# Kernel tuning notes

Measured on AMD Instinct MI355X. Metric: run time of the kernel, lower is better.

The kernel has to match this reference:

```python
import jax, jax.numpy as jnp
import numpy as np
import math

B, S, F, D, H, L, E, K = 8, 1024, 8, 512, 8, 3, 4, 2
HD = D // H


def _ln(x, g, b, eps=1e-5):
    m = x.mean(-1, keepdims=True)
    v = x.var(-1, keepdims=True)
    return (x - m) / jnp.sqrt(v + eps) * g + b


def _pos_encoding(seq, d):
    pos = jnp.arange(seq, dtype=jnp.float32)[:, None]
    div = jnp.exp(jnp.arange(0, d, 2, dtype=jnp.float32) * (-math.log(10000.0) / d))
    pe = jnp.zeros((seq, d), jnp.float32)
    pe = pe.at[:, 0::2].set(jnp.sin(pos * div))
    pe = pe.at[:, 1::2].set(jnp.cos(pos * div))
    return pe


def setup_inputs() -> dict:
    key = jax.random.key(0)
    ks = iter(jax.random.split(key, 40))

    def w(shape, s=0.02):
        return jax.random.normal(next(ks), shape, jnp.float32) * s

    return {
        "x": jax.random.normal(next(ks), (B, S, F), jnp.float32),
        "Wp": w((D, F)), "bp": jnp.zeros((D,), jnp.float32),
        "femb": w((5, D)),
        "qkv_w": w((L, 3 * D, D)), "qkv_b": jnp.zeros((L, 3 * D), jnp.float32),
        "ow": w((L, D, D)), "ob": jnp.zeros((L, D), jnp.float32),
        "g1": jnp.ones((L, D), jnp.float32), "beta1": jnp.zeros((L, D), jnp.float32),
        "gw": w((L, E, D)), "gb": jnp.zeros((L, E), jnp.float32),
        "ew1": w((L, E, 2 * D, D)), "eb1": jnp.zeros((L, E, 2 * D), jnp.float32),
        "ew2": w((L, E, D, 2 * D)), "eb2": jnp.zeros((L, E, D), jnp.float32),
        "g2": jnp.ones((L, D), jnp.float32), "beta2": jnp.zeros((L, D), jnp.float32),
        "hw": w((3, D)), "hb": jnp.zeros((3,), jnp.float32),
        "freq_idx": 2,
    }


def reference(x, Wp, bp, femb, qkv_w, qkv_b, ow, ob, g1, beta1, gw, gb,
              ew1, eb1, ew2, eb2, g2, beta2, hw, hb, freq_idx):
    # instance norm over time axis (torch std is unbiased -> ddof=1)
    mean = x.mean(axis=1, keepdims=True)
    std = x.std(axis=1, ddof=1, keepdims=True) + 1e-5
    xn = (x - mean) / std

    h = xn @ Wp.T + bp                      # [B,S,D]
    h = h + femb[freq_idx]                  # broadcast freq embedding
    h = h + _pos_encoding(S, D)

    for l in range(L):
        # --- multi-head self-attention ---
        qkv = h @ qkv_w[l].T + qkv_b[l]     # [B,S,3D]
        q, k, v = jnp.split(qkv, 3, axis=-1)
        q = q.reshape(B, S, H, HD).transpose(0, 2, 1, 3)
        k = k.reshape(B, S, H, HD).transpose(0, 2, 1, 3)
        v = v.reshape(B, S, H, HD).transpose(0, 2, 1, 3)
        att = jax.nn.softmax(jnp.einsum('bhqd,bhkd->bhqk', q, k) / math.sqrt(HD), axis=-1)
        o = jnp.einsum('bhqk,bhkd->bhqd', att, v).transpose(0, 2, 1, 3).reshape(B, S, D)
        o = o @ ow[l].T + ob[l]
        h = _ln(h + o, g1[l], beta1[l])

        # --- SparseMoE: top-k softmax gating, renormalized combine ---
        flat = h.reshape(-1, D)                               # [T,D], T=B*S
        probs = jax.nn.softmax(flat @ gw[l].T + gb[l], axis=-1)
        tw, ti = jax.lax.top_k(probs, K)                      # [T,K]
        tw = tw / tw.sum(axis=-1, keepdims=True)
        hid = jax.nn.relu(jnp.einsum('td,efd->tef', flat, ew1[l]) + eb1[l])  # [T,E,2D]
        eo = jnp.einsum('tef,edf->ted', hid, ew2[l]) + eb2[l]                # [T,E,D]
        cw = (jax.nn.one_hot(ti, E, dtype=flat.dtype) * tw[..., None]).sum(1)  # [T,E]
        moe = jnp.einsum('te,ted->td', cw, eo).reshape(B, S, D)
        h = _ln(h + moe, g2[l], beta2[l])

    return h[:, -1, :] @ hw.T + hb           # [B,3] quantiles
```

## Files before the change

kernel.cpp:

```cpp
#include <hip/hip_runtime.h>
#include <hip/hip_bf16.h>
#include <math.h>

typedef __hip_bfloat16 bf16;
typedef __attribute__((ext_vector_type(8))) short short8;
typedef __attribute__((ext_vector_type(4))) short s4v;
typedef __attribute__((ext_vector_type(4))) float f32x4;

constexpr int B_ = 8, S_ = 1024, F_ = 8, D_ = 512, H_ = 8, E_ = 4;
constexpr int T_  = B_ * S_;
constexpr int D3_ = 3 * D_;
constexpr int CAP_ = T_ * 2 + E_ * 128;

__device__ __forceinline__ float b2f(bf16 v) { return __bfloat162float(v); }
__device__ __forceinline__ float ldin(const void* p, size_t i, int bf) {
  return bf ? __bfloat162float(((const bf16*)p)[i]) : ((const float*)p)[i];
}
__device__ __forceinline__ void gload16(const void* g, void* l) {
  __builtin_amdgcn_global_load_lds((const __attribute__((address_space(1))) unsigned int*)g,
                                   (__attribute__((address_space(3))) unsigned int*)l, 16, 0, 0);
}

__global__ void detect_kernel(const void* __restrict__ x, int* __restrict__ flag) {
  if (threadIdx.x == 0 && blockIdx.x == 0) {
    const unsigned short* u = (const unsigned short*)x;
    int c = 0;
    for (int i = 0; i < 256; i += 2) {
      int ex = (u[i] >> 7) & 0xFF;
      if (ex >= 96 && ex <= 144) c++;
    }
    flag[0] = (c >= 64) ? 1 : 0;
  }
}

__global__ __launch_bounds__(256) void convw_kernel(const void* __restrict__ Asrc, size_t offA,
                                                    size_t nA,
                                                    const void* __restrict__ Bsrc, size_t offB,
                                                    bf16* __restrict__ dst,
                                                    const int* __restrict__ flag) {
  const int bf = flag[0];
  size_t i = ((size_t)blockIdx.x * 256 + threadIdx.x) * 8;
  const void* s = Asrc;
  size_t so = offA + i;
  if (i >= nA) { s = Bsrc; so = offB + (i - nA); }
  if (bf) {
    *(short8*)(dst + i) = *(const short8*)((const bf16*)s + so);
  } else {
    const float* sp = (const float*)s + so;
    short8 v;
#pragma unroll
    for (int u = 0; u < 8; u++) { bf16 t = __float2bfloat16(sp[u]); v[u] = *(short*)&t; }
    *(short8*)(dst + i) = v;
  }
}

__global__ __launch_bounds__(256) void instnorm_kernel(const void* __restrict__ x,
                                                       float* __restrict__ xn,
                                                       const int* __restrict__ flag) {
  const int bf = flag[0];
  int b = blockIdx.x / F_, f = blockIdx.x % F_;
  int tid = threadIdx.x;
  __shared__ float red[256];
  const int base = b * S_ * F_ + f;
  float s = 0.f;
  for (int j = tid; j < S_; j += 256) s += ldin(x, base + j * F_, bf);
  red[tid] = s; __syncthreads();
  for (int w = 128; w; w >>= 1) { if (tid < w) red[tid] += red[tid + w]; __syncthreads(); }
  float mean = red[0] / S_;
  __syncthreads();
  float v = 0.f;
  for (int j = tid; j < S_; j += 256) { float d = ldin(x, base + j * F_, bf) - mean; v += d * d; }
  red[tid] = v; __syncthreads();
  for (int w = 128; w; w >>= 1) { if (tid < w) red[tid] += red[tid + w]; __syncthreads(); }
  float inv = 1.f / (sqrtf(red[0] / (float)(S_ - 1)) + 1e-5f);
  for (int j = tid; j < S_; j += 256) xn[base + j * F_] = (ldin(x, base + j * F_, bf) - mean) * inv;
}

__global__ __launch_bounds__(256) void pe_kernel(const void* __restrict__ bp,
                                                 const void* __restrict__ femb,
                                                 const int* __restrict__ freq_idx,
                                                 float* __restrict__ addtab,
                                                 const int* __restrict__ flag) {
  const int bf = flag[0];
  int idx = blockIdx.x * 256 + threadIdx.x;
  int dp = idx & (D_ / 2 - 1);
  int s  = idx / (D_ / 2);
  int d0 = dp * 2;
  int fi = freq_idx[0];
  const float cexp = -9.2103403719761836f / (float)D_;
  float ang = (float)s * expf((float)d0 * cexp);
  float sv, cv;
  sincosf(ang, &sv, &cv);
  addtab[(size_t)s * D_ + d0]     = sv + ldin(bp, d0, bf)     + ldin(femb, (size_t)fi * D_ + d0, bf);
  addtab[(size_t)s * D_ + d0 + 1] = cv + ldin(bp, d0 + 1, bf) + ldin(femb, (size_t)fi * D_ + d0 + 1, bf);
}

constexpr int IPG_ = 8;
__global__ __launch_bounds__(256) void input_proj_kernel(const float* __restrict__ xn,
                                                         const void* __restrict__ Wp,
                                                         const float* __restrict__ addtab,
                                                         float* __restrict__ h,
                                                         bf16* __restrict__ hb16,
                                                         const int* __restrict__ flag) {
  const int bf = flag[0];
  const int tid = threadIdx.x;
  const int d0 = tid * 2;
  const int tbase = blockIdx.x * IPG_;
  float wp0[8], wp1[8];
  if (bf) {
    short8 w0 = *(const short8*)((const bf16*)Wp + (size_t)d0 * F_);
    short8 w1 = *(const short8*)((const bf16*)Wp + (size_t)(d0 + 1) * F_);
#pragma unroll
    for (int f = 0; f < 8; f++) {
      unsigned short u0 = (unsigned short)w0[f], u1 = (unsigned short)w1[f];
      wp0[f] = __bfloat162float(*(bf16*)&u0);
      wp1[f] = __bfloat162float(*(bf16*)&u1);
    }
  } else {
    const float* wpf = (const float*)Wp + (size_t)d0 * F_;
    f32x4 a = *(const f32x4*)(wpf);
    f32x4 b = *(const f32x4*)(wpf + 4);
    f32x4 c = *(const f32x4*)(wpf + 8);
    f32x4 d = *(const f32x4*)(wpf + 12);
#pragma unroll
    for (int f = 0; f < 4; f++) { wp0[f] = a[f]; wp0[4 + f] = b[f]; wp1[f] = c[f]; wp1[4 + f] = d[f]; }
  }
#pragma unroll
  for (int g = 0; g < IPG_; g++) {
    int t = tbase + g;
    int s = t & (S_ - 1);
    const float* xr = xn + (size_t)t * F_;
    f32x4 x0 = *(const f32x4*)xr;
    f32x4 x1 = *(const f32x4*)(xr + 4);
    const float2 at = *(const float2*)(addtab + (size_t)s * D_ + d0);
    float a0 = at.x, a1 = at.y;
#pragma unroll
    for (int f = 0; f < 4; f++) { a0 += x0[f] * wp0[f]; a1 += x0[f] * wp1[f]; }
#pragma unroll
    for (int f = 0; f < 4; f++) { a0 += x1[f] * wp0[4 + f]; a1 += x1[f] * wp1[4 + f]; }
    *(float2*)(h + (size_t)t * D_ + d0) = make_float2(a0, a1);
    bf16 b0 = __float2bfloat16(a0), b1 = __float2bfloat16(a1);
    unsigned pk = (unsigned)(*(unsigned short*)&b0) | ((unsigned)(*(unsigned short*)&b1) << 16);
    *(unsigned*)(hb16 + (size_t)t * D_ + d0) = pk;
  }
}

template <int MODE>
__global__ __launch_bounds__(256) void mfma_gemm(
    const bf16* __restrict__ A, const bf16* __restrict__ Wt,
    const void* __restrict__ bias, size_t boff, void* __restrict__ C_,
    int Kd, int lda, int ldb, int ldc, const int* __restrict__ flag) {
  const int wbf = flag[0];
  __shared__ bf16 As[3][128][32];
  __shared__ bf16 Bs[3][128][32];
  const int tid = threadIdx.x;
  const int ln = tid & 63, wv = tid >> 6;
  int id = blockIdx.x + gridDim.x * blockIdx.y;
  int xcd = id & 7, idq = id >> 3;
  const int n0 = (idq % gridDim.x) * 128;
  const int m0 = (xcd + 8 * (idq / gridDim.x)) * 128;
  const int wr = (wv >> 1) * 64, wc = (wv & 1) * 64;
  const int mrow = ln & 15, quad = ln >> 4;
  const int srow = ln >> 2;
  const int skof = (ln & 3) * 8;
  const int kchunk = Kd / gridDim.z;
  const int kbeg = blockIdx.z * kchunk;
  const int kend = kbeg + kchunk;

  auto stage = [&](int pb, int k0) {
#pragma unroll
    for (int j = 0; j < 2; j++) {
      int row = 16 * (4 * j + wv) + srow;
      gload16(A + (size_t)(m0 + row) * lda + k0 + skof,
              (char*)&As[pb][0][0] + (size_t)(4 * j + wv) * 1024);
    }
#pragma unroll
    for (int j = 0; j < 2; j++) {
      int row = 16 * (4 * j + wv) + srow;
      gload16(Wt + (size_t)(n0 + row) * ldb + k0 + skof,
              (char*)&Bs[pb][0][0] + (size_t)(4 * j + wv) * 1024);
    }
  };

  f32x4 acc[4][4];
#pragma unroll
  for (int i = 0; i < 4; i++)
#pragma unroll
    for (int j = 0; j < 4; j++) acc[i][j] = (f32x4){0.f, 0.f, 0.f, 0.f};

  stage(0, kbeg);
  stage(1, kbeg + 32);
  int p = 0;
  for (int k0 = kbeg; k0 < kend; k0 += 32) {
    if (k0 + 32 < kend) asm volatile("s_waitcnt vmcnt(4)" ::: "memory");
    else                asm volatile("s_waitcnt vmcnt(0)" ::: "memory");
    __builtin_amdgcn_s_barrier();
    __builtin_amdgcn_sched_barrier(0);
    short8 af[4], bfr[4];
#pragma unroll
    for (int t = 0; t < 4; t++) {
      af[t]  = *(const short8*)&As[p][wr + t * 16 + mrow][quad * 8];
      bfr[t] = *(const short8*)&Bs[p][wc + t * 16 + mrow][quad * 8];
    }
    if (k0 + 64 < kend) {
      int ps = (p == 0) ? 2 : p - 1;
      stage(ps, k0 + 64);
    }
#pragma unroll
    for (int i = 0; i < 4; i++)
#pragma unroll
      for (int j = 0; j < 4; j++)
        acc[i][j] = __builtin_amdgcn_mfma_f32_16x16x32_bf16(af[i], bfr[j], acc[i][j], 0, 0, 0);
    p = (p == 2) ? 0 : p + 1;
  }

  bf16* slice = (MODE == 0) ? (bf16*)C_ + (size_t)blockIdx.z * T_ * D_ : (bf16*)C_;
#pragma unroll
  for (int tj = 0; tj < 4; tj++) {
    int n = n0 + wc + tj * 16 + mrow;
    float bv = (MODE == 3) ? ldin(bias, boff + n, wbf) : 0.f;
#pragma unroll
    for (int ti = 0; ti < 4; ti++) {
      int mbase = m0 + wr + ti * 16 + quad * 4;
#pragma unroll
      for (int r = 0; r < 4; r++) {
        int m = mbase + r;
        float v = acc[ti][tj][r];
        slice[(size_t)m * ldc + n] = __float2bfloat16(MODE == 3 ? v + bv : v);
      }
    }
  }
}

__global__ __launch_bounds__(256) void attn_kernel(const bf16* __restrict__ qkv,
                                                   bf16* __restrict__ o) {
  __shared__ bf16 QP[64][72];
  __shared__ bf16 Ks[64][72];
  __shared__ bf16 Vt[64][72];
  const int tid = threadIdx.x;
  const int ln = tid & 63, wv = tid >> 6;
  const int mrow = ln & 15, quad = ln >> 4;
  const int id = blockIdx.x;
  const int xcd = id & 7, j = id >> 3;
  const int qt = j & 15;
  const int pr = xcd + 8 * (j >> 4);
  const int hh = pr & 7, b = pr >> 3;
  const int q0 = qt * 64;
  const int sr = tid >> 2;
  const int sg = tid & 3;
  const int sc = sg * 8;

  {
    const bf16* src = qkv + (size_t)(b * S_ + q0 + sr) * D3_ + hh * 64;
    *(short8*)&QP[sr][sc]      = *(const short8*)(src + sc);
    *(short8*)&QP[sr][sc + 32] = *(const short8*)(src + sc + 32);
  }
  __syncthreads();
  short8 aq[2];
  aq[0] = *(const short8*)&QP[wv * 16 + mrow][quad * 8];
  aq[1] = *(const short8*)&QP[wv * 16 + mrow][quad * 8 + 32];

  float m_st = -1e30f, l_st = 0.f;
  f32x4 oacc[4];
#pragma unroll
  for (int t = 0; t < 4; t++) oacc[t] = (f32x4){0.f, 0.f, 0.f, 0.f};

  for (int kt = 0; kt < 16; kt++) {
    int k0 = kt * 64;
    __syncthreads();
    {
      const bf16* src = qkv + (size_t)(b * S_ + k0 + sr) * D3_ + D_ + hh * 64;
      *(short8*)&Ks[sr][sc]      = *(const short8*)(src + sc);
      *(short8*)&Ks[sr][sc + 32] = *(const short8*)(src + sc + 32);
    }
    {
      const bf16* src = qkv + (size_t)(b * S_ + k0 + sr) * D3_ + 2 * D_ + hh * 64;
      short8 v0 = *(const short8*)(src + sc);
      short8 v1 = *(const short8*)(src + sc + 32);
      int col0 = sr ^ (sg << 4);
      int col1 = sr ^ (((sg + 4) & 3) << 4);
#pragma unroll
      for (int u = 0; u < 8; u++) {
        *(short*)&Vt[sc + u][col0]      = v0[u];
        *(short*)&Vt[sc + 32 + u][col1] = v1[u];
      }
    }
    __syncthreads();
    f32x4 s[4];
#pragma unroll
    for (int t = 0; t < 4; t++) {
      s[t] = (f32x4){0.f, 0.f, 0.f, 0.f};
#pragma unroll
      for (int ks = 0; ks < 2; ks++) {
        short8 bk = *(const short8*)&Ks[t * 16 + mrow][quad * 8 + ks * 32];
        s[t] = __builtin_amdgcn_mfma_f32_16x16x32_bf16(bk, aq[ks], s[t], 0, 0, 0);
      }
    }
    float rm = s[0][0];
#pragma unroll
    for (int t = 0; t < 4; t++)
#pragma unroll
      for (int r = 0; r < 4; r++) rm = fmaxf(rm, s[t][r]);
    rm *= 0.125f;
    rm = fmaxf(rm, __shfl_xor(rm, 16, 64));
    rm = fmaxf(rm, __shfl_xor(rm, 32, 64));
    float mnew = fmaxf(m_st, rm);
    float alpha = __expf(m_st - mnew);
    m_st = mnew;
    float rs = 0.f;
#pragma unroll
    for (int t = 0; t < 4; t++) {
      s4v pk;
#pragma unroll
      for (int r = 0; r < 4; r++) {
        float p = __expf(s[t][r] * 0.125f - mnew);
        rs += p;
        bf16 tb = __float2bfloat16(p);
        pk[r] = *(short*)&tb;
      }
      *(s4v*)&QP[wv * 16 + mrow][t * 16 + quad * 4] = pk;
    }
    rs += __shfl_xor(rs, 16, 64);
    rs += __shfl_xor(rs, 32, 64);
    l_st = l_st * alpha + rs;
    float af4[4];
#pragma unroll
    for (int r = 0; r < 4; r++) af4[r] = __shfl(alpha, quad * 4 + r, 64);
#pragma unroll
    for (int t = 0; t < 4; t++)
#pragma unroll
      for (int r = 0; r < 4; r++) oacc[t][r] *= af4[r];
    short8 ap[2];
    ap[0] = *(const short8*)&QP[wv * 16 + mrow][quad * 8];
    ap[1] = *(const short8*)&QP[wv * 16 + mrow][quad * 8 + 32];
#pragma unroll
    for (int t = 0; t < 4; t++) {
      int d = t * 16 + mrow;
      int swz = ((d >> 3) & 3) << 4;
#pragma unroll
      for (int ks = 0; ks < 2; ks++) {
        short8 bv = *(const short8*)&Vt[d][(quad * 8 + ks * 32) ^ swz];
        oacc[t] = __builtin_amdgcn_mfma_f32_16x16x32_bf16(ap[ks], bv, oacc[t], 0, 0, 0);
      }
    }
  }
  float linv[4];
#pragma unroll
  for (int r = 0; r < 4; r++) linv[r] = 1.f / __shfl(l_st, quad * 4 + r, 64);
#pragma unroll
  for (int r = 0; r < 4; r++) {
    size_t base = (size_t)(b * S_ + q0 + wv * 16 + quad * 4 + r) * D_ + hh * 64;
#pragma unroll
    for (int t = 0; t < 4; t++)
      o[base + t * 16 + mrow] = __float2bfloat16(oacc[t][r] * linv[r]);
  }
}

__global__ __launch_bounds__(256) void reduce_ln_kernel(float* __restrict__ h,
                                                        bf16* __restrict__ hb16,
                                                        const bf16* __restrict__ ps,
                                                        int nsl, int mode,
                                                        const void* __restrict__ bias,
                                                        size_t boff,
                                                        const float* __restrict__ cw,
                                                        const void* __restrict__ eb2p,
                                                        size_t e2off,
                                                        const void* __restrict__ g,
                                                        const void* __restrict__ beta,
                                                        size_t off,
                                                        const int* __restrict__ flag) {
  const int bf = flag[0];
  int t = blockIdx.x, tid = threadIdx.x;
  __shared__ float r1[256], r2[256];
  const size_t base = (size_t)t * D_;
  float o0 = 0.f, o1 = 0.f;
  for (int s = 0; s < nsl; s++) {
    o0 += b2f(ps[(size_t)s * T_ * D_ + base + tid]);
    o1 += b2f(ps[(size_t)s * T_ * D_ + base + tid + 256]);
  }
  if (mode == 0) {
    o0 += ldin(bias, boff + tid, bf);
    o1 += ldin(bias, boff + tid + 256, bf);
  } else {
#pragma unroll
    for (int e = 0; e < 4; e++) {
      float w = cw[t * 4 + e];
      o0 += w * ldin(eb2p, e2off + e * D_ + tid, bf);
      o1 += w * ldin(eb2p, e2off + e * D_ + tid + 256, bf);
    }
  }
  float* hr = h + base;
  float v0 = hr[tid] + o0;
  float v1 = hr[tid + 256] + o1;
  r1[tid] = v0 + v1;
  r2[tid] = v0 * v0 + v1 * v1;
  __syncthreads();
  for (int w = 128; w; w >>= 1) { if (tid < w) { r1[tid] += r1[tid + w]; r2[tid] += r2[tid + w]; } __syncthreads(); }
  float mean = r1[0] * (1.f / D_);
  float var  = r2[0] * (1.f / D_) - mean * mean;
  float rstd = rsqrtf(var + 1e-5f);
  float n0 = (v0 - mean) * rstd * ldin(g, off + tid, bf) + ldin(beta, off + tid, bf);
  float n1 = (v1 - mean) * rstd * ldin(g, off + tid + 256, bf) + ldin(beta, off + tid + 256, bf);
  hr[tid] = n0;
  hr[tid + 256] = n1;
  hb16[base + tid] = __float2bfloat16(n0);
  hb16[base + tid + 256] = __float2bfloat16(n1);
}

__global__ __launch_bounds__(256) void gate_kernel(const float* __restrict__ hbuf,
                                                   const void* __restrict__ gw, size_t gwoff,
                                                   const void* __restrict__ gb, size_t gboff,
                                                   float* __restrict__ cw,
                                                   int* __restrict__ einfo,
                                                   float* __restrict__ w0a,
                                                   float* __restrict__ w1a,
                                                   const int* __restrict__ flag) {
  const int bf = flag[0];
  int lane = threadIdx.x & 63, wv = threadIdx.x >> 6;
  int t = blockIdx.x * 4 + wv;
  const float* xr = hbuf + (size_t)t * D_;
  float a[4] = {0, 0, 0, 0};
  for (int d = lane; d < D_; d += 64) {
    float xv = xr[d];
#pragma unroll
    for (int e = 0; e < 4; e++) a[e] += xv * ldin(gw, gwoff + e * D_ + d, bf);
  }
#pragma unroll
  for (int e = 0; e < 4; e++)
    for (int off = 32; off; off >>= 1) a[e] += __shfl_xor(a[e], off, 64);
  if (lane == 0) {
    float lg[4];
#pragma unroll
    for (int e = 0; e < 4; e++) lg[e] = a[e] + ldin(gb, gboff + e, bf);
    float m = fmaxf(fmaxf(lg[0], lg[1]), fmaxf(lg[2], lg[3]));
    float p[4], s = 0.f;
#pragma unroll
    for (int e = 0; e < 4; e++) { p[e] = __expf(lg[e] - m); s += p[e]; }
#pragma unroll
    for (int e = 0; e < 4; e++) p[e] /= s;
    int i0 = 0;
    for (int e = 1; e < 4; e++) if (p[e] > p[i0]) i0 = e;
    int i1 = -1;
    for (int e = 0; e < 4; e++) if (e != i0 && (i1 < 0 || p[e] > p[i1])) i1 = e;
    float s2 = p[i0] + p[i1];
    float ww0 = p[i0] / s2, ww1 = p[i1] / s2;
    float outw[4] = {0, 0, 0, 0};
    outw[i0] = ww0; outw[i1] = ww1;
#pragma unroll
    for (int e = 0; e < 4; e++) cw[t * 4 + e] = outw[e];
    einfo[t] = i0 | (i1 << 4);
    w0a[t] = ww0; w1a[t] = ww1;
  }
}

__global__ __launch_bounds__(256) void route_scan_kernel(const int* __restrict__ einfo,
                                                         int* __restrict__ off,
                                                         int* __restrict__ endp,
                                                         int* __restrict__ cur,
                                                         int* __restrict__ tmap) {
  __shared__ int red[4][256];
  int tid = threadIdx.x;
  int c[4] = {0, 0, 0, 0};
  for (int t = tid; t < T_; t += 256) {
    int inf = einfo[t];
    c[inf & 15]++;
    c[(inf >> 4) & 15]++;
  }
#pragma unroll
  for (int e = 0; e < 4; e++) red[e][tid] = c[e];
  __syncthreads();
  for (int w = 128; w; w >>= 1) {
    if (tid < w)
#pragma unroll
      for (int e = 0; e < 4; e++) red[e][tid] += red[e][tid + w];
    __syncthreads();
  }
  if (tid == 0) {
    int o = 0, idx = 0;
#pragma unroll
    for (int e = 0; e < 4; e++) {
      int cnt = red[e][0];
      off[e] = o;
      endp[e] = o + cnt;
      cur[e] = 0;
      int nt = (cnt + 127) >> 7;
      for (int i = 0; i < nt; i++) tmap[1 + idx++] = e | (i << 8);
      o += nt << 7;
    }
    tmap[0] = idx;
  }
}

__global__ __launch_bounds__(256) void scatter_kernel(const int* __restrict__ einfo,
                                                      const float* __restrict__ w0a,
                                                      const float* __restrict__ w1a,
                                                      const int* __restrict__ off,
                                                      int* __restrict__ cur,
                                                      int* __restrict__ pack,
                                                      float* __restrict__ wlist) {
  int t = blockIdx.x * 256 + threadIdx.x;
  int lane = threadIdx.x & 63;
  int inf = einfo[t];
#pragma unroll
  for (int rank = 0; rank < 2; rank++) {
    int my_e = (rank == 0) ? (inf & 15) : ((inf >> 4) & 15);
    float w = (rank == 0) ? w0a[t] : w1a[t];
#pragma unroll
    for (int e = 0; e < 4; e++) {
      bool p = (my_e == e);
      unsigned long long mask = __ballot(p);
      if (!mask) continue;
      int leader = __ffsll((long long)mask) - 1;
      int base = 0;
      if (lane == leader) base = atomicAdd(&cur[e], (int)__popcll(mask));
      base = __shfl(base, leader, 64);
      if (p) {
        int pos = off[e] + base + (int)__popcll(mask & ((1ULL << lane) - 1ULL));
        pack[pos] = t * 2 + rank;
        wlist[pos] = w;
      }
    }
  }
}

__global__ __launch_bounds__(256) void moe_mat1_kernel(
    const bf16* __restrict__ A, const bf16* __restrict__ Wt,
    const void* __restrict__ bias, size_t boff, bf16* __restrict__ hid,
    const int* __restrict__ off, const int* __restrict__ endp,
    const int* __restrict__ pack, const float* __restrict__ wlist,
    const int* __restrict__ tmap, const int* __restrict__ flag) {
  const int wbf = flag[0];
  int id = blockIdx.x + 8 * blockIdx.y;
  int xcd = id & 7, idq = id >> 3;
  int wx = idq & 7, wy = xcd + 8 * (idq >> 3);
  if (wy >= tmap[0]) return;
  int ent = tmap[1 + wy];
  const int e = ent & 255, mt = ent >> 8;
  const int o = off[e], en = endp[e];
  const int n0 = wx * 128;
  __shared__ bf16 As[3][128][32];
  __shared__ bf16 Bs[3][128][32];
  const int tid = threadIdx.x;
  const int ln = tid & 63, wv = tid >> 6;
  const int m0 = o + mt * 128;
  const int wr = (wv >> 1) * 64, wc = (wv & 1) * 64;
  const int mrow = ln & 15, quad = ln >> 4;
  const int srow = ln >> 2;
  const int skof = (ln & 3) * 8;
  int tokr[2];
#pragma unroll
  for (int j = 0; j < 2; j++) {
    int pos = m0 + 16 * (4 * j + wv) + srow;
    tokr[j] = pack[min(pos, en - 1)] >> 1;
  }
  const size_t wbase = (size_t)e * 1024 * 512;

  auto stage = [&](int pb, int k0) {
#pragma unroll
    for (int j = 0; j < 2; j++)
      gload16(A + (size_t)tokr[j] * 512 + k0 + skof,
              (char*)&As[pb][0][0] + (size_t)(4 * j + wv) * 1024);
#pragma unroll
    for (int j = 0; j < 2; j++) {
      int row = 16 * (4 * j + wv) + srow;
      gload16(Wt + wbase + (size_t)(n0 + row) * 512 + k0 + skof,
              (char*)&Bs[pb][0][0] + (size_t)(4 * j + wv) * 1024);
    }
  };

  f32x4 acc[4][4];
#pragma unroll
  for (int i = 0; i < 4; i++)
#pragma unroll
    for (int j = 0; j < 4; j++) acc[i][j] = (f32x4){0.f, 0.f, 0.f, 0.f};

  stage(0, 0);
  stage(1, 32);
  int p = 0;
  for (int k0 = 0; k0 < 512; k0 += 32) {
    if (k0 + 32 < 512) asm volatile("s_waitcnt vmcnt(4)" ::: "memory");
    else               asm volatile("s_waitcnt vmcnt(0)" ::: "memory");
    __builtin_amdgcn_s_barrier();
    __builtin_amdgcn_sched_barrier(0);
    short8 af[4], bfr[4];
#pragma unroll
    for (int t = 0; t < 4; t++) {
      af[t]  = *(const short8*)&As[p][wr + t * 16 + mrow][quad * 8];
      bfr[t] = *(const short8*)&Bs[p][wc + t * 16 + mrow][quad * 8];
    }
    if (k0 + 64 < 512) {
      int ps = (p == 0) ? 2 : p - 1;
      stage(ps, k0 + 64);
    }
#pragma unroll
    for (int i = 0; i < 4; i++)
#pragma unroll
      for (int j = 0; j < 4; j++)
        acc[i][j] = __builtin_amdgcn_mfma_f32_16x16x32_bf16(af[i], bfr[j], acc[i][j], 0, 0, 0);
    p = (p == 2) ? 0 : p + 1;
  }

#pragma unroll
  for (int ti = 0; ti < 4; ti++) {
#pragma unroll
    for (int r = 0; r < 4; r++) {
      int pos = m0 + wr + ti * 16 + quad * 4 + r;
      float w = (pos < en) ? wlist[pos] : 0.f;
#pragma unroll
      for (int tj = 0; tj < 4; tj++) {
        int ncol = n0 + wc + tj * 16 + mrow;
        float v = acc[ti][tj][r] + ldin(bias, boff + e * 1024 + ncol, wbf);
        hid[(size_t)pos * 1024 + ncol] = __float2bfloat16(fmaxf(v, 0.f) * w);
      }
    }
  }
}

__global__ __launch_bounds__(256) void moe_mat2_kernel(
    const bf16* __restrict__ hid, const bf16* __restrict__ Wt,
    bf16* __restrict__ psl,
    const int* __restrict__ off, const int* __restrict__ endp,
    const int* __restrict__ pack, const int* __restrict__ tmap,
    const int* __restrict__ flag) {
  int id = blockIdx.x + 4 * blockIdx.y;
  int xcd = id & 7, idq = id >> 3;
  int wx = idq & 3, wy = xcd + 8 * (idq >> 2);
  if (wy >= tmap[0]) return;
  int ent = tmap[1 + wy];
  const int e = ent & 255, mt = ent >> 8;
  const int o = off[e], en = endp[e];
  const int n0 = wx * 128;
  __shared__ bf16 As[3][128][32];
  __shared__ bf16 Bs[3][128][32];
  const int tid = threadIdx.x;
  const int ln = tid & 63, wv = tid >> 6;
  const int m0 = o + mt * 128;
  const int wr = (wv >> 1) * 64, wc = (wv & 1) * 64;
  const int mrow = ln & 15, quad = ln >> 4;
  const int srow = ln >> 2;
  const int skof = (ln & 3) * 8;
  const int kbeg = blockIdx.z * 512;
  const size_t wbase = (size_t)e * 512 * 1024;

  auto stage = [&](int pb, int k0) {
#pragma unroll
    for (int j = 0; j < 2; j++) {
      int row = 16 * (4 * j + wv) + srow;
      gload16(hid + (size_t)(m0 + row) * 1024 + k0 + skof,
              (char*)&As[pb][0][0] + (size_t)(4 * j + wv) * 1024);
    }
#pragma unroll
    for (int j = 0; j < 2; j++) {
      int row = 16 * (4 * j + wv) + srow;
      gload16(Wt + wbase + (size_t)(n0 + row) * 1024 + k0 + skof,
              (char*)&Bs[pb][0][0] + (size_t)(4 * j + wv) * 1024);
    }
  };

  f32x4 acc[4][4];
#pragma unroll
  for (int i = 0; i < 4; i++)
#pragma unroll
    for (int j = 0; j < 4; j++) acc[i][j] = (f32x4){0.f, 0.f, 0.f, 0.f};

  stage(0, kbeg);
  stage(1, kbeg + 32);
  int p = 0;
  for (int k0 = kbeg; k0 < kbeg + 512; k0 += 32) {
    if (k0 + 32 < kbeg + 512) asm volatile("s_waitcnt vmcnt(4)" ::: "memory");
    else                      asm volatile("s_waitcnt vmcnt(0)" ::: "memory");
    __builtin_amdgcn_s_barrier();
    __builtin_amdgcn_sched_barrier(0);
    short8 af[4], bfr[4];
#pragma unroll
    for (int t = 0; t < 4; t++) {
      af[t]  = *(const short8*)&As[p][wr + t * 16 + mrow][quad * 8];
      bfr[t] = *(const short8*)&Bs[p][wc + t * 16 + mrow][quad * 8];
    }
    if (k0 + 64 < kbeg + 512) {
      int ps = (p == 0) ? 2 : p - 1;
      stage(ps, k0 + 64);
    }
#pragma unroll
    for (int i = 0; i < 4; i++)
#pragma unroll
      for (int j = 0; j < 4; j++)
        acc[i][j] = __builtin_amdgcn_mfma_f32_16x16x32_bf16(af[i], bfr[j], acc[i][j], 0, 0, 0);
    p = (p == 2) ? 0 : p + 1;
  }

#pragma unroll
  for (int ti = 0; ti < 4; ti++) {
#pragma unroll
    for (int r = 0; r < 4; r++) {
      int pos = m0 + wr + ti * 16 + quad * 4 + r;
      if (pos < en) {
        int pk = pack[pos];
        int tok = pk >> 1, rank = pk & 1;
        bf16* dst = psl + (size_t)(rank * 2 + blockIdx.z) * T_ * D_ + (size_t)tok * D_;
#pragma unroll
        for (int tj = 0; tj < 4; tj++) {
          int ncol = n0 + wc + tj * 16 + mrow;
          dst[ncol] = __float2bfloat16(acc[ti][tj][r]);
        }
      }
    }
  }
}

__global__ __launch_bounds__(256) void head_kernel(const float* __restrict__ hbuf,
                                                   const void* __restrict__ hw,
                                                   const void* __restrict__ hb,
                                                   void* __restrict__ out,
                                                   const int* __restrict__ flag) {
  const int bf = flag[0];
  int bq = blockIdx.x, tid = threadIdx.x;
  int b = bq / 3, q = bq % 3;
  __shared__ float red[256];
  const float* xr = hbuf + (size_t)(b * S_ + (S_ - 1)) * D_;
  float sacc = xr[tid] * ldin(hw, (size_t)q * D_ + tid, bf)
             + xr[tid + 256] * ldin(hw, (size_t)q * D_ + tid + 256, bf);
  red[tid] = sacc; __syncthreads();
  for (int w = 128; w; w >>= 1) { if (tid < w) red[tid] += red[tid + w]; __syncthreads(); }
  if (tid == 0) {
    float r = red[0] + ldin(hb, q, bf);
    if (bf) ((bf16*)out)[bq] = __float2bfloat16(r);
    else    ((float*)out)[bq] = r;
  }
}

extern "C" void kernel_launch(void* const* d_in, const int* in_sizes, int n_in,
                              void* d_out, int out_size, void* d_ws, size_t ws_size,
                              hipStream_t stream) {
  const void* x    = d_in[0];
  const void* Wp   = d_in[1];
  const void* bp   = d_in[2];
  const void* femb = d_in[3];
  const void* qkvw = d_in[4];
  const void* qkvb = d_in[5];
  const void* ow   = d_in[6];
  const void* ob   = d_in[7];
  const void* g1   = d_in[8];
  const void* be1  = d_in[9];
  const void* gw   = d_in[10];
  const void* gb   = d_in[11];
  const void* ew1  = d_in[12];
  const void* eb1  = d_in[13];
  const void* ew2  = d_in[14];
  const void* eb2  = d_in[15];
  const void* g2   = d_in[16];
  const void* be2  = d_in[17];
  const void* hw   = d_in[18];
  const void* hb   = d_in[19];
  const int*  freq = (const int*)d_in[20];

  int*   flag  = (int*)d_ws;
  int*   off   = flag + 64;
  int*   endp  = off + 4;
  int*   cur   = endp + 4;
  int*   einfo = flag + 128;
  float* w0a   = (float*)(einfo + T_);
  float* w1a   = w0a + T_;
  int*   pack  = (int*)(w1a + T_);
  float* wlist = (float*)(pack + CAP_);
  int*   tmap  = (int*)(wlist + CAP_);
  float* xn    = (float*)(tmap + 160);
  float* h     = xn + 65536;
  float* cw    = h + (size_t)T_ * D_;
  bf16*  hb16  = (bf16*)(cw + (size_t)T_ * E_);
  bf16*  R     = hb16 + (size_t)T_ * D_;
  bf16*  qkvb16 = R;
  bf16*  ao    = R + (size_t)T_ * D3_;
  bf16*  hid   = R;
  bf16*  psl   = R + (size_t)CAP_ * 1024;
  bf16*  wcvt  = psl + (size_t)4 * T_ * D_;
  bf16*  wq    = wcvt;
  bf16*  wo    = wcvt + (size_t)D3_ * D_;
  bf16*  we1   = wcvt;
  bf16*  we2   = wcvt + (size_t)E_ * 1024 * 512;
  float* addtab = (float*)R;

  constexpr size_t NQ = (size_t)D3_ * D_;
  constexpr size_t NO = (size_t)D_ * D_;
  constexpr size_t NE = (size_t)E_ * 1024 * 512;

  detect_kernel<<<1, 64, 0, stream>>>(x, flag);
  instnorm_kernel<<<B_ * F_, 256, 0, stream>>>(x, xn, flag);
  pe_kernel<<<(S_ * D_ / 2) / 256, 256, 0, stream>>>(bp, femb, freq, addtab, flag);
  input_proj_kernel<<<T_ / IPG_, 256, 0, stream>>>(xn, Wp, addtab, h, hb16, flag);

  for (int l = 0; l < 3; l++) {
    convw_kernel<<<(NQ + NO) / 2048, 256, 0, stream>>>(
        qkvw, (size_t)l * NQ, NQ, ow, (size_t)l * NO, wcvt, flag);
    mfma_gemm<3><<<dim3(D3_ / 128, T_ / 128), 256, 0, stream>>>(
        hb16, wq, qkvb, (size_t)l * D3_, qkvb16, D_, D_, D_, D3_, flag);
    attn_kernel<<<B_ * H_ * (S_ / 64), 256, 0, stream>>>(qkvb16, ao);
    mfma_gemm<0><<<dim3(D_ / 128, T_ / 128, 2), 256, 0, stream>>>(
        ao, wo, nullptr, 0, psl, D_, D_, D_, D_, flag);
    reduce_ln_kernel<<<T_, 256, 0, stream>>>(
        h, hb16, psl, 2, 0, ob, (size_t)l * D_, nullptr, nullptr, 0,
        g1, be1, (size_t)l * D_, flag);
    gate_kernel<<<T_ / 4, 256, 0, stream>>>(h, gw, (size_t)l * E_ * D_, gb, (size_t)l * E_,
                                            cw, einfo, w0a, w1a, flag);
    route_scan_kernel<<<1, 256, 0, stream>>>(einfo, off, endp, cur, tmap);
    scatter_kernel<<<T_ / 256, 256, 0, stream>>>(einfo, w0a, w1a, off, cur, pack, wlist);
    convw_kernel<<<(NE + NE) / 2048, 256, 0, stream>>>(
        ew1, (size_t)l * NE, NE, ew2, (size_t)l * NE, wcvt, flag);
    moe_mat1_kernel<<<dim3(8, 136), 256, 0, stream>>>(
        hb16, we1, eb1, (size_t)l * E_ * 1024, hid,
        off, endp, pack, wlist, tmap, flag);
    moe_mat2_kernel<<<dim3(4, 136, 2), 256, 0, stream>>>(
        hid, we2, psl, off, endp, pack, tmap, flag);
    reduce_ln_kernel<<<T_, 256, 0, stream>>>(
        h, hb16, psl, 4, 1, nullptr, 0, cw, eb2, (size_t)l * E_ * D_,
        g2, be2, (size_t)l * D_, flag);
  }

  head_kernel<<<24, 256, 0, stream>>>(h, hw, hb, d_out, flag);
}
```

Baseline: 850.3 us.

## Prefetch next K/V tile into registers and raise MFMA wave priority in attention

The attention kernel now loads the next K and V tile from global memory into registers while the current tile is being computed, then writes it to LDS at the top of the next iteration. This is meant to hide global-load latency behind the MFMA work. The __syncthreads calls are replaced with raw s_barrier plus an explicit lgkmcnt wait, and s_setprio brackets the MFMA loops. It costs extra registers, which may lower occupancy, and relies on the manual barriers and waits being correct for the LDS hazards.

```diff
diff --git a/kernel.cpp b/kernel.cpp
--- a/kernel.cpp
+++ b/kernel.cpp
@@ -249,6 +249,8 @@
   const int sr = tid >> 2;
   const int sg = tid & 3;
   const int sc = sg * 8;
+  const int col0 = sr ^ (sg << 4);
+  const int col1 = sr ^ (((sg + 4) & 3) << 4);
 
   {
     const bf16* src = qkv + (size_t)(b * S_ + q0 + sr) * D3_ + hh * 64;
@@ -265,28 +267,39 @@
 #pragma unroll
   for (int t = 0; t < 4; t++) oacc[t] = (f32x4){0.f, 0.f, 0.f, 0.f};
 
+  short8 kA, kB, vA, vB;
+  {
+    const bf16* srcK = qkv + (size_t)(b * S_ + sr) * D3_ + D_ + hh * 64;
+    kA = *(const short8*)(srcK + sc);
+    kB = *(const short8*)(srcK + sc + 32);
+    const bf16* srcV = qkv + (size_t)(b * S_ + sr) * D3_ + 2 * D_ + hh * 64;
+    vA = *(const short8*)(srcV + sc);
+    vB = *(const short8*)(srcV + sc + 32);
+  }
+
   for (int kt = 0; kt < 16; kt++) {
-    int k0 = kt * 64;
-    __syncthreads();
-    {
-      const bf16* src = qkv + (size_t)(b * S_ + k0 + sr) * D3_ + D_ + hh * 64;
-      *(short8*)&Ks[sr][sc]      = *(const short8*)(src + sc);
-      *(short8*)&Ks[sr][sc + 32] = *(const short8*)(src + sc + 32);
-    }
-    {
-      const bf16* src = qkv + (size_t)(b * S_ + k0 + sr) * D3_ + 2 * D_ + hh * 64;
-      short8 v0 = *(const short8*)(src + sc);
-      short8 v1 = *(const short8*)(src + sc + 32);
-      int col0 = sr ^ (sg << 4);
-      int col1 = sr ^ (((sg + 4) & 3) << 4);
-#pragma unroll
-      for (int u = 0; u < 8; u++) {
-        *(short*)&Vt[sc + u][col0]      = v0[u];
-        *(short*)&Vt[sc + 32 + u][col1] = v1[u];
-      }
-    }
-    __syncthreads();
+    __builtin_amdgcn_s_barrier();
+    *(short8*)&Ks[sr][sc]      = kA;
+    *(short8*)&Ks[sr][sc + 32] = kB;
+#pragma unroll
+    for (int u = 0; u < 8; u++) {
+      *(short*)&Vt[sc + u][col0]      = vA[u];
+      *(short*)&Vt[sc + 32 + u][col1] = vB[u];
+    }
+    if (kt + 1 < 16) {
+      int k0n = (kt + 1) * 64;
+      const bf16* srcK = qkv + (size_t)(b * S_ + k0n + sr) * D3_ + D_ + hh * 64;
+      kA = *(const short8*)(srcK + sc);
+      kB = *(const short8*)(srcK + sc + 32);
+      const bf16* srcV = qkv + (size_t)(b * S_ + k0n + sr) * D3_ + 2 * D_ + hh * 64;
+      vA = *(const short8*)(srcV + sc);
+      vB = *(const short8*)(srcV + sc + 32);
+    }
+    asm volatile("s_waitcnt lgkmcnt(0)" ::: "memory");
+    __builtin_amdgcn_s_barrier();
+    __builtin_amdgcn_sched_barrier(0);
     f32x4 s[4];
+    __builtin_amdgcn_s_setprio(1);
 #pragma unroll
     for (int t = 0; t < 4; t++) {
       s[t] = (f32x4){0.f, 0.f, 0.f, 0.f};
@@ -296,6 +309,7 @@
         s[t] = __builtin_amdgcn_mfma_f32_16x16x32_bf16(bk, aq[ks], s[t], 0, 0, 0);
       }
     }
+    __builtin_amdgcn_s_setprio(0);
     float rm = s[0][0];
 #pragma unroll
     for (int t = 0; t < 4; t++)
@@ -333,6 +347,7 @@
     short8 ap[2];
     ap[0] = *(const short8*)&QP[wv * 16 + mrow][quad * 8];
     ap[1] = *(const short8*)&QP[wv * 16 + mrow][quad * 8 + 32];
+    __builtin_amdgcn_s_setprio(1);
 #pragma unroll
     for (int t = 0; t < 4; t++) {
       int d = t * 16 + mrow;
@@ -343,6 +358,7 @@
         oacc[t] = __builtin_amdgcn_mfma_f32_16x16x32_bf16(ap[ks], bv, oacc[t], 0, 0, 0);
       }
     }
+    __builtin_amdgcn_s_setprio(0);
   }
   float linv[4];
 #pragma unroll
```

After: 844.5 us. Within noise of the previous version (-0.7%).
